# Kernel optimization log

Measured on AMD Instinct MI355X. Metric: run time of the kernel, lower is better.

The kernel has to match this reference:

```python
import jax, jax.numpy as jnp
import numpy as np

HIDDEN = 1024

def setup_inputs() -> dict:
    key = jax.random.key(0)
    ks = jax.random.split(key, 8)
    s = 1.0 / np.sqrt(HIDDEN)
    return {
        "query": jax.random.normal(ks[0], (8, 1024, HIDDEN), dtype=jnp.float32),
        "ref": jax.random.normal(ks[1], (8, 4096, HIDDEN), dtype=jnp.float32),
        "Wq": jax.random.normal(ks[2], (HIDDEN, HIDDEN), dtype=jnp.float32) * s,
        "bq": jax.random.normal(ks[3], (HIDDEN,), dtype=jnp.float32) * s,
        "Wk": jax.random.normal(ks[4], (HIDDEN, HIDDEN), dtype=jnp.float32) * s,
        "bk": jax.random.normal(ks[5], (HIDDEN,), dtype=jnp.float32) * s,
        "Wv": jax.random.normal(ks[6], (HIDDEN, HIDDEN), dtype=jnp.float32) * s,
        "bv": jax.random.normal(ks[7], (HIDDEN,), dtype=jnp.float32) * s,
    }

def reference(query, ref, Wq, bq, Wk, bk, Wv, bv):
    norm_fact = 1.0 / np.sqrt(HIDDEN).astype(np.float32)
    Q = query @ Wq + bq            # [B, Lq, H]
    K = ref @ Wk + bk              # [B, Lk, H]
    V = ref @ Wv + bv              # [B, Lk, H]
    scores = jnp.einsum('bqh,bkh->bqk', Q, K)  # NOTE: unscaled logits (faithful to source)
    attn = jax.nn.softmax(scores, axis=-1) * norm_fact  # post-softmax scale
    return jnp.einsum('bqk,bkh->bqh', attn, V)
```

## Files before the change

kernel.cpp:

```cpp
#include <hip/hip_runtime.h>

typedef _Float16 f16x8 __attribute__((ext_vector_type(8)));
typedef float    f32x4 __attribute__((ext_vector_type(4)));
typedef unsigned short ushort_t;

__device__ __forceinline__ ushort_t f2h(float x) {
    union { _Float16 h; ushort_t u; } c; c.h = (_Float16)x; return c.u;
}

typedef __attribute__((address_space(1))) void gvoid;
typedef __attribute__((address_space(3))) void lvoid;
__device__ __forceinline__ void g2l16(const ushort_t* g, ushort_t* l) {
    __builtin_amdgcn_global_load_lds((gvoid*)g, (lvoid*)l, 16, 0, 0);
}

#define BM 128
#define BN 128
#define BK 32
#define NT 256

__global__ void wconv_kernel(const float* __restrict__ Wq, const float* __restrict__ Wk,
                             const float* __restrict__ Wv,
                             ushort_t* __restrict__ tq, ushort_t* __restrict__ tk,
                             ushort_t* __restrict__ tv) {
    const int z = blockIdx.z;
    const float* W = (z == 0) ? Wq : (z == 1) ? Wk : Wv;
    ushort_t* T = (z == 0) ? tq : (z == 1) ? tk : tv;
    const int n  = blockIdx.x * blockDim.x + threadIdx.x;
    const int kb = blockIdx.y * 128;
    for (int k0 = kb; k0 < kb + 128; k0 += 8) {
        union { ushort_t u[8]; uint4 v; } H;
        #pragma unroll
        for (int e = 0; e < 8; ++e)
            H.u[e] = f2h(W[(long long)(k0 + e) * 1024 + n]);
        *(uint4*)&T[(long long)n * 1024 + k0] = H.v;
    }
}

__global__ void aconv_kernel(const float* __restrict__ x, ushort_t* __restrict__ h, int n4) {
    int i = blockIdx.x * blockDim.x + threadIdx.x;
    if (i >= n4) return;
    float4 v = ((const float4*)x)[i];
    union { ushort_t u[4]; uint2 w; } H;
    H.u[0] = f2h(v.x); H.u[1] = f2h(v.y); H.u[2] = f2h(v.z); H.u[3] = f2h(v.w);
    ((uint2*)h)[i] = H.w;
}

__global__ void add2_kernel(const float4* __restrict__ a, const float4* __restrict__ b,
                            float4* __restrict__ o, int n4) {
    int i = blockIdx.x * blockDim.x + threadIdx.x;
    if (i >= n4) return;
    float4 x = a[i], y = b[i];
    float4 r;
    r.x = x.x + y.x; r.y = x.y + y.y; r.z = x.z + y.z; r.w = x.w + y.w;
    o[i] = r;
}

template<int OUT_MODE, bool BIAS, int NSPLIT>
__global__ __launch_bounds__(NT, 2)
void gemm_kernel(const ushort_t* __restrict__ A, const ushort_t* __restrict__ B,
                 const float* __restrict__ bias,
                 float* __restrict__ Cf, ushort_t* __restrict__ Ch,
                 int K, int lda, int ldb, int ldc,
                 long long sA, long long sB, long long sC, int tM)
{
    __shared__ __align__(16) ushort_t As[BM * BK];
    __shared__ __align__(16) ushort_t Bs[BN * BK];
    __shared__ float biasS[BN];

    const int tid  = threadIdx.x;
    const int zz   = blockIdx.z;
    const int b    = zz / NSPLIT;
    const int kc   = zz % NSPLIT;
    const int m0   = blockIdx.y * BM;
    const int n0   = blockIdx.x * BN;
    const int lane = tid & 63;
    const int w    = tid >> 6;
    const int wm   = (w >> 1) * 64;
    const int wn   = (w & 1) * 64;
    const int l15  = lane & 15;
    const int quad = lane >> 4;

    if (OUT_MODE == 0 && NSPLIT > 1)
        Cf += (long long)kc * (long long)tM;

    if (BIAS && tid < BN) biasS[tid] = bias[n0 + tid];

    const long long aBase = (long long)b * sA + (long long)m0 * lda;
    const long long bBase = (long long)b * sB + (long long)n0 * ldb;

    f32x4 acc[4][4];
    #pragma unroll
    for (int i = 0; i < 4; ++i)
        #pragma unroll
        for (int j = 0; j < 4; ++j)
            #pragma unroll
            for (int r = 0; r < 4; ++r) acc[i][j][r] = 0.0f;

    const int kBeg = kc * K;
    const int kEnd = kBeg + K;
    for (int k0 = kBeg; k0 < kEnd; k0 += BK) {
        __syncthreads();
        {
            const int row = tid >> 2;
            const int col = (tid & 3) * 8;
            const int lds = (tid & ~63) * 8;
            g2l16(A + aBase + (long long)row * lda + k0 + col, &As[lds]);
            g2l16(B + bBase + (long long)row * ldb + k0 + col, &Bs[lds]);
            const int row2 = row + 64;
            const int lds2 = lds + NT * 8;
            g2l16(A + aBase + (long long)row2 * lda + k0 + col, &As[lds2]);
            g2l16(B + bBase + (long long)row2 * ldb + k0 + col, &Bs[lds2]);
        }
        __syncthreads();

        f16x8 af[4], bf[4];
        #pragma unroll
        for (int i = 0; i < 4; ++i)
            af[i] = *(const f16x8*)&As[(wm + i * 16 + l15) * BK + quad * 8];
        #pragma unroll
        for (int j = 0; j < 4; ++j)
            bf[j] = *(const f16x8*)&Bs[(wn + j * 16 + l15) * BK + quad * 8];
        #pragma unroll
        for (int i = 0; i < 4; ++i)
            #pragma unroll
            for (int j = 0; j < 4; ++j)
                acc[i][j] = __builtin_amdgcn_mfma_f32_16x16x32_f16(af[i], bf[j], acc[i][j], 0, 0, 0);
    }

    #pragma unroll
    for (int i = 0; i < 4; ++i)
        #pragma unroll
        for (int j = 0; j < 4; ++j) {
            const int row0 = wm + i * 16 + quad * 4;
            const int col  = wn + j * 16 + l15;
            float c[4];
            #pragma unroll
            for (int r = 0; r < 4; ++r) {
                c[r] = acc[i][j][r];
                if (BIAS) c[r] += biasS[col];
            }
            if constexpr (OUT_MODE == 0) {
                #pragma unroll
                for (int r = 0; r < 4; ++r)
                    Cf[(long long)b * sC + (long long)(m0 + row0 + r) * ldc + (n0 + col)] = c[r];
            } else if constexpr (OUT_MODE == 1) {
                #pragma unroll
                for (int r = 0; r < 4; ++r)
                    Ch[(long long)b * sC + (long long)(m0 + row0 + r) * ldc + (n0 + col)] = f2h(c[r]);
            } else {
                const int mg  = m0 + row0;
                const int bb  = mg / tM;
                const int key = mg % tM;
                union { ushort_t u[4]; uint2 v; } P;
                #pragma unroll
                for (int r = 0; r < 4; ++r) P.u[r] = f2h(c[r]);
                *(uint2*)&Ch[(long long)bb * sC + (long long)(n0 + col) * ldc + key] = P.v;
            }
        }
}

__global__ void softmax_kernel(const float* __restrict__ S, ushort_t* __restrict__ P) {
    const int row  = blockIdx.x;
    const int tid  = threadIdx.x;
    const int lane = tid & 63;
    const int wid  = tid >> 6;
    const float* s = S + (long long)row * 4096;
    float4 v[4];
    float m = -3.4e38f;
    #pragma unroll
    for (int i = 0; i < 4; ++i) {
        v[i] = ((const float4*)s)[tid + i * 256];
        m = fmaxf(fmaxf(fmaxf(m, v[i].x), fmaxf(v[i].y, v[i].z)), v[i].w);
    }
    __shared__ float redm[4], reds[4];
    #pragma unroll
    for (int o = 32; o > 0; o >>= 1) m = fmaxf(m, __shfl_down(m, o));
    if (lane == 0) redm[wid] = m;
    __syncthreads();
    m = fmaxf(fmaxf(redm[0], redm[1]), fmaxf(redm[2], redm[3]));
    float sum = 0.f;
    #pragma unroll
    for (int i = 0; i < 4; ++i) {
        v[i].x = __expf(v[i].x - m); v[i].y = __expf(v[i].y - m);
        v[i].z = __expf(v[i].z - m); v[i].w = __expf(v[i].w - m);
        sum += v[i].x + v[i].y + v[i].z + v[i].w;
    }
    #pragma unroll
    for (int o = 32; o > 0; o >>= 1) sum += __shfl_down(sum, o);
    if (lane == 0) reds[wid] = sum;
    __syncthreads();
    sum = reds[0] + reds[1] + reds[2] + reds[3];
    const float scale = 0.03125f / sum;
    ushort_t* p = P + (long long)row * 4096;
    #pragma unroll
    for (int i = 0; i < 4; ++i) {
        union { ushort_t u[4]; uint2 w; } Pk;
        Pk.u[0] = f2h(v[i].x * scale); Pk.u[1] = f2h(v[i].y * scale);
        Pk.u[2] = f2h(v[i].z * scale); Pk.u[3] = f2h(v[i].w * scale);
        ((uint2*)p)[tid + i * 256] = Pk.w;
    }
}

extern "C" void kernel_launch(void* const* d_in, const int* in_sizes, int n_in,
                              void* d_out, int out_size, void* d_ws, size_t ws_size,
                              hipStream_t stream) {
    const float* query = (const float*)d_in[0];
    const float* ref   = (const float*)d_in[1];
    const float* Wq    = (const float*)d_in[2];
    const float* bq    = (const float*)d_in[3];
    const float* Wk    = (const float*)d_in[4];
    const float* bk    = (const float*)d_in[5];
    const float* Wv    = (const float*)d_in[6];
    const float* bv    = (const float*)d_in[7];
    float* out = (float*)d_out;
    (void)in_sizes; (void)n_in; (void)out_size; (void)ws_size;

    char* ws = (char*)d_ws;
    float*    S   = (float*)ws;
    ushort_t* Qa  = (ushort_t*)ws;
    ushort_t* Ra  = (ushort_t*)(ws + 16777216);
    ushort_t* Qp  = (ushort_t*)(ws + 134217728);
    ushort_t* Kp  = (ushort_t*)(ws + 150994944);
    ushort_t* Vt  = (ushort_t*)(ws + 218103808);
    ushort_t* WqT = (ushort_t*)(ws + 282066944);
    ushort_t* WkT = (ushort_t*)(ws + 284164096);
    ushort_t* WvT = (ushort_t*)(ws + 286261248);
    ushort_t* P   = Kp;
    float*    Ppart = (float*)ws;

    wconv_kernel<<<dim3(4, 8, 3), 256, 0, stream>>>(Wq, Wk, Wv, WqT, WkT, WvT);
    aconv_kernel<<<8192, 256, 0, stream>>>(query, Qa, 2097152);
    aconv_kernel<<<32768, 256, 0, stream>>>(ref, Ra, 8388608);

    gemm_kernel<1, true, 1><<<dim3(8, 64, 1), NT, 0, stream>>>(
        Qa, WqT, bq, nullptr, Qp, 1024, 1024, 1024, 1024, 0, 0, 0, 0);
    gemm_kernel<1, true, 1><<<dim3(8, 256, 1), NT, 0, stream>>>(
        Ra, WkT, bk, nullptr, Kp, 1024, 1024, 1024, 1024, 0, 0, 0, 0);
    gemm_kernel<3, true, 1><<<dim3(8, 256, 1), NT, 0, stream>>>(
        Ra, WvT, bv, nullptr, Vt, 1024, 1024, 1024, 4096, 0, 0, 4194304LL, 4096);

    gemm_kernel<0, false, 1><<<dim3(32, 8, 8), NT, 0, stream>>>(
        Qp, Kp, nullptr, S, nullptr, 1024, 1024, 1024, 4096,
        1048576LL, 4194304LL, 4194304LL, 0);

    softmax_kernel<<<8192, 256, 0, stream>>>(S, P);

    gemm_kernel<0, false, 2><<<dim3(8, 8, 16), NT, 0, stream>>>(
        P, Vt, nullptr, Ppart, nullptr, 2048, 4096, 4096, 1024,
        4194304LL, 4194304LL, 1048576LL, 8388608);

    add2_kernel<<<8192, 256, 0, stream>>>(
        (const float4*)Ppart, (const float4*)(Ppart + 8388608), (float4*)out, 2097152);
}
```

Before: 737.0 us.

## Add 256x256-tile pipelined MFMA GEMM kernel for the large projections and attention matmuls

Adds a new GEMM kernel with 256x256 output tiles, 512 threads, BK=64, and double-buffered LDS filled by direct global-to-LDS loads into an XOR-swizzled layout. Each K-tile is split into four phases that interleave fragment loads, async staging of the next tile, and MFMA bursts raised in priority with s_setprio. Fine-grained vmcnt waits and barriers set the schedule. The K/V projections, QK^T and PV GEMMs switch to this kernel to get more operand reuse per tile and better overlap of memory with compute. The cost is 128KB of LDS per block, heavy register pressure, and fewer blocks in flight, which may hurt occupancy or tail balance on the smaller grids.

```diff
diff --git a/kernel.cpp b/kernel.cpp
--- a/kernel.cpp
+++ b/kernel.cpp
@@ -160,6 +160,193 @@
         }
 }
 
+__device__ __forceinline__ f16x8 ldfrag(const ushort_t* base, int row, int ks, int quad) {
+    int byte_ = (row << 7) + (ks << 6) + (quad << 4);
+    byte_ ^= (row & 7) << 4;
+    return *(const f16x8*)((const char*)base + byte_);
+}
+
+template<int OUT_MODE, bool BIAS, int NSPLIT>
+__global__ __launch_bounds__(512, 2)
+void gemm256_kernel(const ushort_t* __restrict__ A, const ushort_t* __restrict__ B,
+                    const float* __restrict__ bias,
+                    float* __restrict__ Cf, ushort_t* __restrict__ Ch,
+                    int K, int lda, int ldb, int ldc,
+                    long long sA, long long sB, long long sC, int tM)
+{
+    __shared__ __align__(16) ushort_t As[2][256 * 64];
+    __shared__ __align__(16) ushort_t Bs[2][256 * 64];
+
+    const int tid  = threadIdx.x;
+    const int lane = tid & 63;
+    const int wid  = tid >> 6;
+    const int wr   = wid >> 2;
+    const int wc   = wid & 3;
+    const int quad = lane >> 4;
+    const int l15  = lane & 15;
+
+    const int zz = blockIdx.z;
+    const int b  = zz / NSPLIT;
+    const int kc = zz % NSPLIT;
+    const int m0 = blockIdx.y * 256;
+    const int n0 = blockIdx.x * 256;
+
+    const ushort_t* Ab = A + (long long)b * sA + (long long)m0 * lda;
+    const ushort_t* Bb = B + (long long)b * sB + (long long)n0 * ldb;
+
+    float* Cfp = Cf;
+    if (OUT_MODE == 0 && NSPLIT > 1) Cfp = Cf + (long long)kc * (long long)tM;
+
+    const int NTILES = K >> 6;
+    const int kBeg   = kc * K;
+    const int tlast  = NTILES - 1;
+
+    const int srow = (wid << 3) + (lane >> 3);
+    const int scol = ((lane & 7) ^ ((lane >> 3) & 7)) << 3;
+
+#define STAGE_A(bf, r0, kcol) g2l16(Ab + (long long)((r0) + srow) * lda + (kcol) + scol, \
+                                    &As[bf][((r0) + (wid << 3)) << 6])
+#define STAGE_B(bf, r0, kcol) g2l16(Bb + (long long)((r0) + srow) * ldb + (kcol) + scol, \
+                                    &Bs[bf][((r0) + (wid << 3)) << 6])
+#define BAR()  __builtin_amdgcn_s_barrier()
+#define SB0()  __builtin_amdgcn_sched_barrier(0)
+#define VMCNT(n) asm volatile("s_waitcnt vmcnt(" #n ")" ::: "memory")
+
+    f32x4 acc[8][4];
+    #pragma unroll
+    for (int i = 0; i < 8; ++i)
+        #pragma unroll
+        for (int j = 0; j < 4; ++j)
+            #pragma unroll
+            for (int r = 0; r < 4; ++r) acc[i][j][r] = 0.0f;
+
+    {
+        const int k0 = kBeg, k1 = kBeg + 64;
+        STAGE_B(0, 0,   k0); STAGE_B(0, 64,  k0);
+        STAGE_B(0, 128, k0); STAGE_B(0, 192, k0);
+        STAGE_A(0, 0,   k0); STAGE_A(0, 128, k0);
+        STAGE_A(0, 64,  k0); STAGE_A(0, 192, k0);
+        STAGE_B(1, 0,   k1); STAGE_B(1, 64,  k1);
+        STAGE_B(1, 128, k1); STAGE_B(1, 192, k1);
+        STAGE_A(1, 0,   k1); STAGE_A(1, 128, k1);
+        VMCNT(8);
+        BAR(); SB0();
+    }
+
+    const int arow = wr * 128 + l15;
+    const int brow = wc * 64 + l15;
+    f16x8 bfr[4][2], afr[2][2];
+
+#define PHASE_AFR(bf, q) \
+    afr[0][0] = ldfrag(&As[bf][0], arow + (q)*32,      0, quad); \
+    afr[0][1] = ldfrag(&As[bf][0], arow + (q)*32,      1, quad); \
+    afr[1][0] = ldfrag(&As[bf][0], arow + (q)*32 + 16, 0, quad); \
+    afr[1][1] = ldfrag(&As[bf][0], arow + (q)*32 + 16, 1, quad);
+
+#define PHASE_MFMA(q) \
+    _Pragma("unroll") \
+    for (int m2 = 0; m2 < 2; ++m2) \
+        _Pragma("unroll") \
+        for (int j = 0; j < 4; ++j) { \
+            acc[(q)*2+m2][j] = __builtin_amdgcn_mfma_f32_16x16x32_f16(afr[m2][0], bfr[j][0], acc[(q)*2+m2][j], 0, 0, 0); \
+            acc[(q)*2+m2][j] = __builtin_amdgcn_mfma_f32_16x16x32_f16(afr[m2][1], bfr[j][1], acc[(q)*2+m2][j], 0, 0, 0); \
+        }
+
+#define TILE_BODY(bf, kn1, kn2) { \
+     \
+    _Pragma("unroll") \
+    for (int j = 0; j < 4; ++j) { \
+        bfr[j][0] = ldfrag(&Bs[bf][0], brow + j*16, 0, quad); \
+        bfr[j][1] = ldfrag(&Bs[bf][0], brow + j*16, 1, quad); \
+    } \
+    PHASE_AFR(bf, 0); \
+    STAGE_A((bf) ^ 1, 64, kn1); STAGE_A((bf) ^ 1, 192, kn1); \
+    BAR(); __builtin_amdgcn_s_setprio(1); \
+    PHASE_MFMA(0); \
+    __builtin_amdgcn_s_setprio(0); BAR(); SB0(); \
+     \
+    PHASE_AFR(bf, 1); \
+    STAGE_B(bf, 0, kn2); STAGE_B(bf, 64, kn2); \
+    BAR(); __builtin_amdgcn_s_setprio(1); \
+    PHASE_MFMA(1); \
+    __builtin_amdgcn_s_setprio(0); VMCNT(10); BAR(); SB0(); \
+     \
+    PHASE_AFR(bf, 2); \
+    STAGE_B(bf, 128, kn2); STAGE_B(bf, 192, kn2); \
+    BAR(); __builtin_amdgcn_s_setprio(1); \
+    PHASE_MFMA(2); \
+    __builtin_amdgcn_s_setprio(0); BAR(); SB0(); \
+     \
+    PHASE_AFR(bf, 3); \
+    STAGE_A(bf, 0, kn2); STAGE_A(bf, 128, kn2); \
+    BAR(); __builtin_amdgcn_s_setprio(1); \
+    PHASE_MFMA(3); \
+    __builtin_amdgcn_s_setprio(0); VMCNT(8); BAR(); SB0(); \
+}
+
+    for (int t = 0; t < NTILES; t += 2) {
+        {
+            const int kn1 = kBeg + (((t + 1) < NTILES ? (t + 1) : tlast) << 6);
+            const int kn2 = kBeg + (((t + 2) < NTILES ? (t + 2) : tlast) << 6);
+            TILE_BODY(0, kn1, kn2);
+        }
+        {
+            const int kn1 = kBeg + (((t + 2) < NTILES ? (t + 2) : tlast) << 6);
+            const int kn2 = kBeg + (((t + 3) < NTILES ? (t + 3) : tlast) << 6);
+            TILE_BODY(1, kn1, kn2);
+        }
+    }
+
+    VMCNT(0);
+
+    float biasv[4];
+    if (BIAS) {
+        #pragma unroll
+        for (int j = 0; j < 4; ++j)
+            biasv[j] = bias[n0 + wc * 64 + j * 16 + l15];
+    }
+
+    #pragma unroll
+    for (int mi = 0; mi < 8; ++mi) {
+        const int row0 = wr * 128 + mi * 16 + quad * 4;
+        #pragma unroll
+        for (int j = 0; j < 4; ++j) {
+            const int col = wc * 64 + j * 16 + l15;
+            float c[4];
+            #pragma unroll
+            for (int r = 0; r < 4; ++r) {
+                c[r] = acc[mi][j][r];
+                if (BIAS) c[r] += biasv[j];
+            }
+            if constexpr (OUT_MODE == 0) {
+                #pragma unroll
+                for (int r = 0; r < 4; ++r)
+                    Cfp[(long long)b * sC + (long long)(m0 + row0 + r) * ldc + (n0 + col)] = c[r];
+            } else if constexpr (OUT_MODE == 1) {
+                #pragma unroll
+                for (int r = 0; r < 4; ++r)
+                    Ch[(long long)b * sC + (long long)(m0 + row0 + r) * ldc + (n0 + col)] = f2h(c[r]);
+            } else {
+                const int mg  = m0 + row0;
+                const int bb2 = mg / tM;
+                const int key = mg % tM;
+                union { ushort_t u[4]; uint2 v; } Pp;
+                #pragma unroll
+                for (int r = 0; r < 4; ++r) Pp.u[r] = f2h(c[r]);
+                *(uint2*)&Ch[(long long)bb2 * sC + (long long)(n0 + col) * ldc + key] = Pp.v;
+            }
+        }
+    }
+#undef STAGE_A
+#undef STAGE_B
+#undef BAR
+#undef SB0
+#undef VMCNT
+#undef PHASE_AFR
+#undef PHASE_MFMA
+#undef TILE_BODY
+}
+
 __global__ void softmax_kernel(const float* __restrict__ S, ushort_t* __restrict__ P) {
     const int row  = blockIdx.x;
     const int tid  = threadIdx.x;
@@ -235,18 +422,18 @@
 
     gemm_kernel<1, true, 1><<<dim3(8, 64, 1), NT, 0, stream>>>(
         Qa, WqT, bq, nullptr, Qp, 1024, 1024, 1024, 1024, 0, 0, 0, 0);
-    gemm_kernel<1, true, 1><<<dim3(8, 256, 1), NT, 0, stream>>>(
+    gemm256_kernel<1, true, 1><<<dim3(4, 128, 1), 512, 0, stream>>>(
         Ra, WkT, bk, nullptr, Kp, 1024, 1024, 1024, 1024, 0, 0, 0, 0);
-    gemm_kernel<3, true, 1><<<dim3(8, 256, 1), NT, 0, stream>>>(
+    gemm256_kernel<3, true, 1><<<dim3(4, 128, 1), 512, 0, stream>>>(
         Ra, WvT, bv, nullptr, Vt, 1024, 1024, 1024, 4096, 0, 0, 4194304LL, 4096);
 
-    gemm_kernel<0, false, 1><<<dim3(32, 8, 8), NT, 0, stream>>>(
+    gemm256_kernel<0, false, 1><<<dim3(16, 4, 8), 512, 0, stream>>>(
         Qp, Kp, nullptr, S, nullptr, 1024, 1024, 1024, 4096,
         1048576LL, 4194304LL, 4194304LL, 0);
 
     softmax_kernel<<<8192, 256, 0, stream>>>(S, P);
 
-    gemm_kernel<0, false, 2><<<dim3(8, 8, 16), NT, 0, stream>>>(
+    gemm256_kernel<0, false, 2><<<dim3(4, 4, 16), 512, 0, stream>>>(
         P, Vt, nullptr, Ppart, nullptr, 2048, 4096, 4096, 1024,
         4194304LL, 4194304LL, 1048576LL, 8388608);
 
```

Result: faster. 640.0 us (-13.2%).
